# Optimization experiments

Hardware: AMD Instinct MI355X
Metric: run time of the kernel (lower is better)

## Reference

```python
import jax, jax.numpy as jnp
import numpy as np

S = 128            # image_size
NF = 64            # nf (channels)
B, N = 16, 1
DIM = S * S // 16  # 1024
HEADS = max(1, S // 16)  # 8
DH = DIM // HEADS  # 128


def setup_inputs() -> dict:
    key = jax.random.key(0)
    ks = jax.random.split(key, 10)
    sc = lambda fan_in: 1.0 / np.sqrt(fan_in)
    return {
        "x": jax.random.normal(ks[0], (B, N, NF, S, S), dtype=jnp.float32),
        "We": jax.random.uniform(ks[1], (DIM, S * S), jnp.float32, -sc(S * S), sc(S * S)),
        "be": jax.random.uniform(ks[2], (DIM,), jnp.float32, -sc(S * S), sc(S * S)),
        "pos": jax.random.normal(ks[3], (1, NF, DIM), dtype=jnp.float32),
        "Wq": jax.random.uniform(ks[4], (DIM, DIM), jnp.float32, -sc(DIM), sc(DIM)),
        "Wk": jax.random.uniform(ks[5], (NF, NF), jnp.float32, -sc(NF), sc(NF)),
        "Wv": jax.random.uniform(ks[6], (DIM, DIM), jnp.float32, -sc(DIM), sc(DIM)),
        "Wo": jax.random.uniform(ks[7], (S * S, DIM), jnp.float32, -sc(DIM), sc(DIM)),
        "bo": jax.random.uniform(ks[8], (S * S,), jnp.float32, -sc(DIM), sc(DIM)),
    }


def reference(x, We, be, pos, Wq, Wk, Wv, Wo, bo):
    b, n, C, H, W = x.shape
    bn = b * n
    xf = x.reshape(bn, C, H * W)                       # [BN, C, S^2]
    xe = jnp.einsum('bcp,dp->bcd', xf, We) + be + pos  # [BN, C, DIM]
    # q projection -> heads -> avgpool over head dim (AvgPool1d(dh) == mean)
    q = jnp.einsum('bcd,ed->bce', xe, Wq).reshape(bn, C, HEADS, DH)
    q = q.transpose(0, 2, 1, 3)                        # [BN, H, C, dh]
    q = q.mean(axis=-1)                                # [BN, H, C]
    k = jax.nn.sigmoid(jnp.einsum('bhc,fc->bhf', q, Wk))  # [BN, H, C]
    v = jnp.einsum('bcd,ed->bce', xe, Wv).reshape(bn, C, HEADS, DH)
    v = v.transpose(0, 2, 1, 3)                        # [BN, H, C, dh]
    # diag_embed(k) @ v == per-channel elementwise scale
    out = k[..., None] * v                             # [BN, H, C, dh]
    out = out.transpose(0, 2, 1, 3).reshape(bn, C, DIM)
    out = jnp.einsum('bcd,pd->bcp', out, Wo) + bo      # [BN, C, S^2]
    return out.reshape(b, n, C, H, W)
```

## Files before the change

### kernel.cpp

```cpp
#include <hip/hip_runtime.h>
#include <cstdint>
#include <cmath>


typedef __attribute__((ext_vector_type(8))) short short8;
typedef __attribute__((ext_vector_type(4))) float f32x4;

#define DIMD 1024
#define NCH  64
#define NHEAD 8
#define DHEAD 128

typedef __attribute__((address_space(1))) unsigned int gu32;
typedef __attribute__((address_space(3))) unsigned int lu32;

__device__ __forceinline__ void gload_lds16(const void* g, void* l) {
  __builtin_amdgcn_global_load_lds((gu32*)g, (lu32*)l, 16, 0, 0);
}

__device__ __forceinline__ unsigned short f2bf(float f) {
  union { float f; unsigned u; } a; a.f = f;
  unsigned u = a.u;
  unsigned r = (u + 0x7fffu + ((u >> 16) & 1u)) >> 16;
  return (unsigned short)r;
}
__device__ __forceinline__ float bf2f(unsigned short h) {
  union { unsigned u; float f; } a; a.u = ((unsigned)h) << 16; return a.f;
}

__device__ __forceinline__ void cvt8_body(const float* __restrict__ in,
                                          unsigned short* __restrict__ out, int i) {
  const float4* p = (const float4*)in + (size_t)i * 2;
  float4 f0 = p[0], f1 = p[1];
  uint4 u;
  u.x = (unsigned)f2bf(f0.x) | ((unsigned)f2bf(f0.y) << 16);
  u.y = (unsigned)f2bf(f0.z) | ((unsigned)f2bf(f0.w) << 16);
  u.z = (unsigned)f2bf(f1.x) | ((unsigned)f2bf(f1.y) << 16);
  u.w = (unsigned)f2bf(f1.z) | ((unsigned)f2bf(f1.w) << 16);
  ((uint4*)out)[i] = u;
}

__global__ __launch_bounds__(256) void cvt_bf16_kernel(
    const float* __restrict__ in, unsigned short* __restrict__ out, int n8) {
  int i = blockIdx.x * 256 + threadIdx.x;
  if (i >= n8) return;
  cvt8_body(in, out, i);
}

__global__ __launch_bounds__(256) void prep_fused(
    const float* __restrict__ x,  unsigned short* __restrict__ x_bf,
    const float* __restrict__ We, unsigned short* __restrict__ We_bf,
    const float* __restrict__ Wo, unsigned short* __restrict__ Wo_bf,
    const float* __restrict__ Wv, unsigned short* __restrict__ Wv_bf,
    const float* __restrict__ Wq, float* __restrict__ wqm) {
  int b = blockIdx.x;
  if (b < 8192) {
    cvt8_body(x, x_bf, b * 256 + threadIdx.x);
  } else if (b < 16384) {
    cvt8_body(We, We_bf, (b - 8192) * 256 + threadIdx.x);
  } else if (b < 24576) {
    cvt8_body(Wo, Wo_bf, (b - 16384) * 256 + threadIdx.x);
  } else if (b < 25088) {
    cvt8_body(Wv, Wv_bf, (b - 24576) * 256 + threadIdx.x);
  } else {
    int bb = b - 25088;
    int h = bb >> 3, dbase = (bb & 7) * 128;
    int d = threadIdx.x & 127, eh = threadIdx.x >> 7;
    const float* p = Wq + ((size_t)(h * DHEAD + eh * 64)) * DIMD + dbase + d;
    float s = 0.f;
    #pragma unroll 8
    for (int e = 0; e < 64; ++e) s += p[(size_t)e * DIMD];
    __shared__ float red[2][128];
    red[eh][d] = s;
    __syncthreads();
    if (eh == 0)
      wqm[h * DIMD + dbase + d] = (red[0][d] + red[1][d]) * (1.0f / DHEAD);
  }
}

__global__ __launch_bounds__(256) void wqm2_kernel(
    const float* __restrict__ Wq, float* __restrict__ wqm) {
  int h = blockIdx.x >> 3, dbase = (blockIdx.x & 7) * 128;
  int d = threadIdx.x & 127, eh = threadIdx.x >> 7;
  const float* p = Wq + ((size_t)(h * DHEAD + eh * 64)) * DIMD + dbase + d;
  float s = 0.f;
  #pragma unroll 8
  for (int e = 0; e < 64; ++e) s += p[(size_t)e * DIMD];
  __shared__ float red[2][128];
  red[eh][d] = s;
  __syncthreads();
  if (eh == 0)
    wqm[h * DIMD + dbase + d] = (red[0][d] + red[1][d]) * (1.0f / DHEAD);
}

__global__ __launch_bounds__(256) void qk2_kernel(
    const unsigned short* __restrict__ xe, const float* __restrict__ wqm,
    const float* __restrict__ Wk, float* __restrict__ kout) {
  int b = blockIdx.x, h = blockIdx.y;
  int c = threadIdx.x & 63, dq = threadIdx.x >> 6;
  __shared__ float red[64][4];
  __shared__ float qs[64];
  const uint4* xr = (const uint4*)(xe + ((size_t)(b * NCH + c)) * DIMD + dq * 256);
  const float* wr = wqm + h * DIMD + dq * 256;
  float s = 0.f;
  #pragma unroll 4
  for (int i = 0; i < 32; ++i) {
    uint4 v = xr[i];
    s += bf2f((unsigned short)(v.x & 0xffff)) * wr[i * 8 + 0];
    s += bf2f((unsigned short)(v.x >> 16))    * wr[i * 8 + 1];
    s += bf2f((unsigned short)(v.y & 0xffff)) * wr[i * 8 + 2];
    s += bf2f((unsigned short)(v.y >> 16))    * wr[i * 8 + 3];
    s += bf2f((unsigned short)(v.z & 0xffff)) * wr[i * 8 + 4];
    s += bf2f((unsigned short)(v.z >> 16))    * wr[i * 8 + 5];
    s += bf2f((unsigned short)(v.w & 0xffff)) * wr[i * 8 + 6];
    s += bf2f((unsigned short)(v.w >> 16))    * wr[i * 8 + 7];
  }
  red[c][dq] = s;
  __syncthreads();
  if (dq == 0) qs[c] = red[c][0] + red[c][1] + red[c][2] + red[c][3];
  __syncthreads();
  int f = c;
  float s2 = 0.f;
  #pragma unroll
  for (int i = 0; i < 16; ++i) {
    int cc = dq * 16 + i;
    s2 += qs[cc] * Wk[f * NCH + cc];
  }
  red[f][dq] = s2;
  __syncthreads();
  if (dq == 0) {
    float q = red[f][0] + red[f][1] + red[f][2] + red[f][3];
    kout[(b * NHEAD + h) * NCH + f] = 1.f / (1.f + expf(-q));
  }
}


#define BARR asm volatile("s_barrier" ::: "memory")
#define VMW(n) asm volatile("s_waitcnt vmcnt(" #n ")" ::: "memory")
#define ENDPH do { \
  asm volatile("s_waitcnt lgkmcnt(0)" ::: "memory"); \
  __builtin_amdgcn_sched_barrier(0); \
  BARR; } while (0)

#define SA(bb, kk, u) gload_lds16(gA + (size_t)(u) * 64 * K + (kk), \
                                  lA0 + (bb) * 16384 + (u) * 4096)
#define SB(bb, kk, u) gload_lds16(gB + (size_t)(u) * 64 * K + (kk), \
                                  lB0 + (bb) * 16384 + (u) * 4096)

#define PH(QM, QN, LOADA, STG) do { \
  if (LOADA) { \
    const unsigned short* ap = &As[buf][wm * 128 + (QM) * 64 + rl][0]; \
    _Pragma("unroll") \
    for (int i = 0; i < 4; ++i) { \
      af0[i] = *(const short8*)(ap + i * 1024 + ((q ^ swz) << 3)); \
      af1[i] = *(const short8*)(ap + i * 1024 + (((4 | q) ^ swz) << 3)); \
    } \
  } \
  const unsigned short* bp = &Bs[buf][wn * 64 + (QN) * 32 + rl][0]; \
  short8 b00 = *(const short8*)(bp + ((q ^ swz) << 3)); \
  short8 b01 = *(const short8*)(bp + 1024 + ((q ^ swz) << 3)); \
  short8 b10 = *(const short8*)(bp + (((4 | q) ^ swz) << 3)); \
  short8 b11 = *(const short8*)(bp + 1024 + (((4 | q) ^ swz) << 3)); \
  STG; \
  BARR; \
  __builtin_amdgcn_s_setprio(1); \
  _Pragma("unroll") \
  for (int i = 0; i < 4; ++i) { \
    acc[(QM)*4+i][(QN)*2+0] = __builtin_amdgcn_mfma_f32_16x16x32_bf16(af0[i], b00, acc[(QM)*4+i][(QN)*2+0], 0, 0, 0); \
    acc[(QM)*4+i][(QN)*2+0] = __builtin_amdgcn_mfma_f32_16x16x32_bf16(af1[i], b10, acc[(QM)*4+i][(QN)*2+0], 0, 0, 0); \
    acc[(QM)*4+i][(QN)*2+1] = __builtin_amdgcn_mfma_f32_16x16x32_bf16(af0[i], b01, acc[(QM)*4+i][(QN)*2+1], 0, 0, 0); \
    acc[(QM)*4+i][(QN)*2+1] = __builtin_amdgcn_mfma_f32_16x16x32_bf16(af1[i], b11, acc[(QM)*4+i][(QN)*2+1], 0, 0, 0); \
  } \
  __builtin_amdgcn_s_setprio(0); \
  ENDPH; \
} while (0)

template<int MODE, int LAYOUT>
__global__ __launch_bounds__(512, 2) void gemm8(
    const unsigned short* __restrict__ A, const unsigned short* __restrict__ Bg,
    float* __restrict__ C, const float* __restrict__ bias,
    int M, int N, int K, int Ksub)
{
  __shared__ __align__(16) unsigned short As[2][256][64];
  __shared__ __align__(16) unsigned short Bs[2][256][64];

  const int bid = blockIdx.x;
  int m0, n0, kz;
  if (LAYOUT == 1) {
    kz = (bid & 7) | (((bid >> 3) & 1) << 3);
    int r = bid >> 4; n0 = (r & 3) * 256; m0 = (r >> 2) * 256;
  } else {
    int nlo = bid & 7; int r = bid >> 3;
    m0 = (r & 3) * 256; n0 = (nlo + 8 * (r >> 2)) * 256; kz = 0;
  }
  const int kbeg = kz * Ksub;
  const int NT = Ksub >> 6;

  const int tid  = threadIdx.x;
  const int lane = tid & 63, wave = tid >> 6;
  const int wm = wave >> 2, wn = wave & 3;
  const int q = lane >> 4, rl = lane & 15;
  const int swz = rl & 7;

  const int srow = wave * 8 + (lane >> 3);
  const int kswz = ((lane & 7) ^ (lane >> 3)) << 3;
  const unsigned short* gA = A  + (size_t)(m0 + srow) * K + kbeg + kswz;
  const unsigned short* gB = Bg + (size_t)(n0 + srow) * K + kbeg + kswz;
  unsigned short* lA0 = &As[0][0][0] + wave * 512;
  unsigned short* lB0 = &Bs[0][0][0] + wave * 512;

  f32x4 acc[8][4] = {};
  short8 af0[4], af1[4];

  SA(0, 0, 0); SA(0, 0, 2);
  SB(0, 0, 0); SB(0, 0, 1); SB(0, 0, 2); SB(0, 0, 3);
  SA(0, 0, 1); SA(0, 0, 3);
  VMW(2);
  BARR;

  for (int t = 0; t < NT; ++t) {
    const int buf = t & 1;
    const int nb = buf ^ 1;
    const bool s = (t + 1) < NT;
    const size_t kn = (size_t)(t + 1) * 64;

    PH(0, 0, true,  if (s) { SB(nb, kn, 0); SB(nb, kn, 1); });
    PH(0, 1, false, if (s) { SB(nb, kn, 2); SB(nb, kn, 3); VMW(4); } else VMW(0));
    PH(1, 0, true,  if (s) { SA(nb, kn, 0); SA(nb, kn, 2); });
    PH(1, 1, false, if (s) { SA(nb, kn, 1); SA(nb, kn, 3); VMW(2); });
  }

  const size_t zoff = (MODE == 3) ? (size_t)kz * (size_t)M * (size_t)N : 0;
  #pragma unroll
  for (int mi = 0; mi < 8; ++mi) {
    #pragma unroll
    for (int nj = 0; nj < 4; ++nj) {
      #pragma unroll
      for (int r = 0; r < 4; ++r) {
        int row = m0 + wm * 128 + mi * 16 + q * 4 + r;
        int col = n0 + wn * 64 + nj * 16 + rl;
        if (MODE == 3) {
          C[zoff + (size_t)row * N + col] = acc[mi][nj][r];
        } else {
          C[(size_t)row * N + col] = acc[mi][nj][r] + bias[col];
        }
      }
    }
  }
}

template<int MODE, int LAYOUT>
__global__ __launch_bounds__(256) void gemm_db(
    const unsigned short* __restrict__ A, const unsigned short* __restrict__ B,
    float* __restrict__ C, const float* __restrict__ bias,
    int M, int N, int K, int Ksub)
{
  __shared__ __align__(16) unsigned short As[2][128][32];
  __shared__ __align__(16) unsigned short Bs[2][128][32];

  const int bid = blockIdx.x;
  int m0, n0, kz;
  if (LAYOUT == 0) {
    kz = bid & 7; int r = bid >> 3; n0 = (r & 7) * 128; m0 = (r >> 3) * 128;
  } else if (LAYOUT == 1) {
    kz = (bid & 7) | (((bid >> 3) & 1) << 3);
    int r = bid >> 4; n0 = (r & 7) * 128; m0 = (r >> 3) * 128;
  } else {
    int nlo = bid & 7, nhi = bid >> 6;
    m0 = ((bid >> 3) & 7) * 128; n0 = (nlo + 8 * nhi) * 128; kz = 0;
  }

  const int tid  = threadIdx.x;
  const int lane = tid & 63, wave = tid >> 6;
  const int kbeg = kz * Ksub;
  const int lrow = lane >> 2;
  const int lcol = (lane & 3) * 8;
  const int q = lane >> 4, rl = lane & 15;
  const int wr = (wave >> 1) * 64, wc = (wave & 1) * 64;

  const unsigned short* ga = A + (size_t)(m0 + wave * 32 + lrow) * K + kbeg + lcol;
  const unsigned short* gb = B + (size_t)(n0 + wave * 32 + lrow) * K + kbeg + lcol;

  f32x4 acc[4][4] = {};

  gload_lds16(ga,                  &As[0][wave * 32][0]);
  gload_lds16(ga + (size_t)16 * K, &As[0][wave * 32 + 16][0]);
  gload_lds16(gb,                  &Bs[0][wave * 32][0]);
  gload_lds16(gb + (size_t)16 * K, &Bs[0][wave * 32 + 16][0]);
  ga += 32; gb += 32;

  int p = 0;
  for (int k0 = 0; k0 < Ksub; k0 += 32) {
    __syncthreads();
    if (k0 + 32 < Ksub) {
      gload_lds16(ga,                  &As[p ^ 1][wave * 32][0]);
      gload_lds16(ga + (size_t)16 * K, &As[p ^ 1][wave * 32 + 16][0]);
      gload_lds16(gb,                  &Bs[p ^ 1][wave * 32][0]);
      gload_lds16(gb + (size_t)16 * K, &Bs[p ^ 1][wave * 32 + 16][0]);
      ga += 32; gb += 32;
    }

    short8 af[4], bf[4];
    #pragma unroll
    for (int i = 0; i < 4; ++i)
      af[i] = *(const short8*)&As[p][wr + i * 16 + rl][q * 8];
    #pragma unroll
    for (int j = 0; j < 4; ++j)
      bf[j] = *(const short8*)&Bs[p][wc + j * 16 + rl][q * 8];
    #pragma unroll
    for (int i = 0; i < 4; ++i)
      #pragma unroll
      for (int j = 0; j < 4; ++j)
        acc[i][j] = __builtin_amdgcn_mfma_f32_16x16x32_bf16(af[i], bf[j], acc[i][j], 0, 0, 0);

    p ^= 1;
  }

  const size_t zoff = (MODE == 3) ? (size_t)kz * (size_t)M * (size_t)N : 0;
  #pragma unroll
  for (int i = 0; i < 4; ++i) {
    #pragma unroll
    for (int j = 0; j < 4; ++j) {
      #pragma unroll
      for (int r = 0; r < 4; ++r) {
        int row = m0 + wr + i * 16 + q * 4 + r;
        int col = n0 + wc + j * 16 + rl;
        if (MODE == 3) {
          C[zoff + (size_t)row * N + col] = acc[i][j][r];
        } else {
          C[(size_t)row * N + col] = acc[i][j][r] + bias[col];
        }
      }
    }
  }
}

template<int NS>
__global__ __launch_bounds__(256) void reduce1_kernel(
    const float* __restrict__ part, const float* __restrict__ be,
    const float* __restrict__ pos, unsigned short* __restrict__ xe) {
  int i = blockIdx.x * 256 + threadIdx.x;
  size_t base = (size_t)i * 4;
  int row = i >> 8, col = (i & 255) * 4;
  float4 s = {0.f, 0.f, 0.f, 0.f};
  #pragma unroll
  for (int sk = 0; sk < NS; ++sk) {
    float4 p = *(const float4*)(part + (size_t)sk * (DIMD * DIMD) + base);
    s.x += p.x; s.y += p.y; s.z += p.z; s.w += p.w;
  }
  float4 bv = *(const float4*)(be + col);
  float4 pv = *(const float4*)(pos + (size_t)(row & 63) * DIMD + col);
  uint2 u;
  u.x = (unsigned)f2bf(s.x + bv.x + pv.x) | ((unsigned)f2bf(s.y + bv.y + pv.y) << 16);
  u.y = (unsigned)f2bf(s.z + bv.z + pv.z) | ((unsigned)f2bf(s.w + bv.w + pv.w) << 16);
  *(uint2*)(xe + base) = u;
}

template<int NS>
__global__ __launch_bounds__(256) void reduce2_kernel(
    const float* __restrict__ part, const float* __restrict__ kv,
    unsigned short* __restrict__ t) {
  int i = blockIdx.x * 256 + threadIdx.x;
  size_t base = (size_t)i * 4;
  int row = i >> 8, col = (i & 255) * 4;
  float4 s = {0.f, 0.f, 0.f, 0.f};
  #pragma unroll
  for (int sk = 0; sk < NS; ++sk) {
    float4 p = *(const float4*)(part + (size_t)sk * (DIMD * DIMD) + base);
    s.x += p.x; s.y += p.y; s.z += p.z; s.w += p.w;
  }
  float sc = kv[((row >> 6) * NHEAD + (col >> 7)) * NCH + (row & 63)];
  uint2 u;
  u.x = (unsigned)f2bf(s.x * sc) | ((unsigned)f2bf(s.y * sc) << 16);
  u.y = (unsigned)f2bf(s.z * sc) | ((unsigned)f2bf(s.w * sc) << 16);
  *(uint2*)(t + base) = u;
}

template<int MODE, bool ABF16, int BM, int BN>
__global__ __launch_bounds__(256) void gemm_bt(
    const void* __restrict__ Ap, const float* __restrict__ B,
    void* __restrict__ C, const float* __restrict__ bias,
    const float* __restrict__ posp, const float* __restrict__ ksc,
    int M, int N, int K)
{
  constexpr int BK = 32;
  constexpr int LDR = BK + 8;
  __shared__ __align__(16) unsigned short As[BM][LDR];
  __shared__ __align__(16) unsigned short Bs[BN][LDR];

  const int tid = threadIdx.x;
  const int m0 = blockIdx.y * BM;
  const int n0 = blockIdx.x * BN;
  constexpr int EA = BM * BK / 256;
  constexpr int EB = BN * BK / 256;
  constexpr int MI = BM / 32;
  constexpr int NI = BN / 32;
  const int lane = tid & 63, wave = tid >> 6;
  const int wr = (wave >> 1) * (BM / 2);
  const int wc = (wave & 1) * (BN / 2);
  const int q = lane >> 4, rl = lane & 15;

  f32x4 acc[MI][NI] = {};

  for (int k0 = 0; k0 < K; k0 += BK) {
    {
      constexpr int CPR = BK / EA;
      int row = tid / CPR;
      int cs  = (tid % CPR) * EA;
      if (ABF16) {
        const unsigned short* a = (const unsigned short*)Ap + (size_t)(m0 + row) * K + k0 + cs;
        #pragma unroll
        for (int v = 0; v < EA / 8; ++v)
          *(uint4*)&As[row][cs + v * 8] = *(const uint4*)(a + v * 8);
      } else {
        const float* a = (const float*)Ap + (size_t)(m0 + row) * K + k0 + cs;
        #pragma unroll
        for (int v = 0; v < EA / 8; ++v) {
          float4 f0 = *(const float4*)(a + v * 8);
          float4 f1 = *(const float4*)(a + v * 8 + 4);
          uint4 u;
          u.x = (unsigned)f2bf(f0.x) | ((unsigned)f2bf(f0.y) << 16);
          u.y = (unsigned)f2bf(f0.z) | ((unsigned)f2bf(f0.w) << 16);
          u.z = (unsigned)f2bf(f1.x) | ((unsigned)f2bf(f1.y) << 16);
          u.w = (unsigned)f2bf(f1.z) | ((unsigned)f2bf(f1.w) << 16);
          *(uint4*)&As[row][cs + v * 8] = u;
        }
      }
    }
    {
      constexpr int CPR = BK / EB;
      int row = tid / CPR;
      int cs  = (tid % CPR) * EB;
      const float* b = B + (size_t)(n0 + row) * K + k0 + cs;
      #pragma unroll
      for (int v = 0; v < EB / 8; ++v) {
        float4 f0 = *(const float4*)(b + v * 8);
        float4 f1 = *(const float4*)(b + v * 8 + 4);
        uint4 u;
        u.x = (unsigned)f2bf(f0.x) | ((unsigned)f2bf(f0.y) << 16);
        u.y = (unsigned)f2bf(f0.z) | ((unsigned)f2bf(f0.w) << 16);
        u.z = (unsigned)f2bf(f1.x) | ((unsigned)f2bf(f1.y) << 16);
        u.w = (unsigned)f2bf(f1.z) | ((unsigned)f2bf(f1.w) << 16);
        *(uint4*)&Bs[row][cs + v * 8] = u;
      }
    }
    __syncthreads();

    short8 af[MI], bf[NI];
    #pragma unroll
    for (int i = 0; i < MI; ++i)
      af[i] = *(const short8*)&As[wr + i * 16 + rl][q * 8];
    #pragma unroll
    for (int j = 0; j < NI; ++j)
      bf[j] = *(const short8*)&Bs[wc + j * 16 + rl][q * 8];
    #pragma unroll
    for (int i = 0; i < MI; ++i)
      #pragma unroll
      for (int j = 0; j < NI; ++j)
        acc[i][j] = __builtin_amdgcn_mfma_f32_16x16x32_bf16(af[i], bf[j], acc[i][j], 0, 0, 0);

    __syncthreads();
  }

  #pragma unroll
  for (int i = 0; i < MI; ++i) {
    #pragma unroll
    for (int j = 0; j < NI; ++j) {
      #pragma unroll
      for (int r = 0; r < 4; ++r) {
        int row = m0 + wr + i * 16 + q * 4 + r;
        int col = n0 + wc + j * 16 + rl;
        float v = acc[i][j][r];
        if (MODE == 0) {
          v += bias[col] + posp[(size_t)(row & 63) * DIMD + col];
          ((unsigned short*)C)[(size_t)row * N + col] = f2bf(v);
        } else if (MODE == 1) {
          v *= ksc[((row >> 6) * NHEAD + (col >> 7)) * NCH + (row & 63)];
          ((unsigned short*)C)[(size_t)row * N + col] = f2bf(v);
        } else {
          ((float*)C)[(size_t)row * N + col] = v + bias[col];
        }
      }
    }
  }
}

__global__ void wqm_kernel(const float* __restrict__ Wq, float* __restrict__ wqm) {
  int h = blockIdx.x;
  for (int d = threadIdx.x; d < DIMD; d += 256) {
    float s = 0.f;
    const float* p = Wq + (size_t)h * DHEAD * DIMD + d;
    #pragma unroll 4
    for (int e = 0; e < DHEAD; ++e) s += p[(size_t)e * DIMD];
    wqm[h * DIMD + d] = s * (1.0f / DHEAD);
  }
}
__global__ void qk_kernel(const unsigned short* __restrict__ xe,
                          const float* __restrict__ wqm,
                          const float* __restrict__ Wk,
                          float* __restrict__ kout) {
  int b = blockIdx.x;
  __shared__ float qs[NHEAD][NCH];
  for (int t = threadIdx.x; t < NHEAD * NCH; t += 256) {
    int h = t >> 6, c = t & 63;
    const unsigned short* xr = xe + (size_t)(b * NCH + c) * DIMD;
    const float* wr = wqm + h * DIMD;
    float s = 0.f;
    #pragma unroll 8
    for (int d = 0; d < DIMD; ++d) s += bf2f(xr[d]) * wr[d];
    qs[h][c] = s;
  }
  __syncthreads();
  for (int t = threadIdx.x; t < NHEAD * NCH; t += 256) {
    int h = t >> 6, f = t & 63;
    float s = 0.f;
    #pragma unroll
    for (int c = 0; c < NCH; ++c) s += qs[h][c] * Wk[f * NCH + c];
    kout[b * (NHEAD * NCH) + h * NCH + f] = 1.f / (1.f + expf(-s));
  }
}

extern "C" void kernel_launch(void* const* d_in, const int* in_sizes, int n_in,
                              void* d_out, int out_size, void* d_ws, size_t ws_size,
                              hipStream_t stream) {
  const float* x   = (const float*)d_in[0];
  const float* We  = (const float*)d_in[1];
  const float* be  = (const float*)d_in[2];
  const float* pos = (const float*)d_in[3];
  const float* Wq  = (const float*)d_in[4];
  const float* Wk  = (const float*)d_in[5];
  const float* Wv  = (const float*)d_in[6];
  const float* Wo  = (const float*)d_in[7];
  const float* bo  = (const float*)d_in[8];
  float* out = (float*)d_out;

  const size_t MB = 1u << 20;
  const size_t WS16 = 102 * MB + 64 * 1024;
  const size_t WS8  = 70 * MB + 64 * 1024;

  if (ws_size >= WS16) {
    char* ws = (char*)d_ws;
    unsigned short* We_bf = (unsigned short*)(ws + 0);
    unsigned short* Wo_bf = (unsigned short*)(ws + 32 * MB);
    unsigned short* x_bf  = (unsigned short*)(ws + 64 * MB);
    unsigned short* Wv_bf = (unsigned short*)(ws + 96 * MB);
    unsigned short* xe    = (unsigned short*)(ws + 98 * MB);
    unsigned short* t     = (unsigned short*)(ws + 100 * MB);
    float* wqm = (float*)(ws + 102 * MB);
    float* kv  = (float*)(ws + 102 * MB + 32 * 1024);

    float* part1 = (float*)d_out;
    float* part2 = (float*)d_out;

    prep_fused<<<dim3(25152), 256, 0, stream>>>(
        x, x_bf, We, We_bf, Wo, Wo_bf, Wv, Wv_bf, Wq, wqm);

    gemm8<3, 1><<<dim3(256), 512, 0, stream>>>(
        x_bf, We_bf, part1, nullptr, 1024, 1024, 16384, 1024);
    reduce1_kernel<16><<<dim3(1024), 256, 0, stream>>>(part1, be, pos, xe);

    qk2_kernel<<<dim3(16, 8), 256, 0, stream>>>(xe, wqm, Wk, kv);

    gemm_db<3, 0><<<dim3(512), 256, 0, stream>>>(
        xe, Wv_bf, part2, nullptr, 1024, 1024, 1024, 128);
    reduce2_kernel<8><<<dim3(1024), 256, 0, stream>>>(part2, kv, t);

    gemm8<2, 2><<<dim3(256), 512, 0, stream>>>(
        t, Wo_bf, out, bo, 1024, 16384, 1024, 1024);
  } else if (ws_size >= WS8) {
    char* ws = (char*)d_ws;
    unsigned short* We_bf = (unsigned short*)(ws + 0);
    unsigned short* Wo_bf = (unsigned short*)(ws + 32 * MB);
    unsigned short* Wv_bf = (unsigned short*)(ws + 64 * MB);
    unsigned short* xe    = (unsigned short*)(ws + 66 * MB);
    unsigned short* t     = (unsigned short*)(ws + 68 * MB);
    float* wqm = (float*)(ws + 70 * MB);
    float* kv  = (float*)(ws + 70 * MB + 32 * 1024);

    char* ob = (char*)d_out;
    unsigned short* x_bf  = (unsigned short*)(ob + 0);
    float* part1 = (float*)(ob + 32 * MB);
    float* part2 = (float*)(ob + 0);

    cvt_bf16_kernel<<<dim3(8192), 256, 0, stream>>>(x,  x_bf,  16777216 / 8);
    cvt_bf16_kernel<<<dim3(8192), 256, 0, stream>>>(We, We_bf, 16777216 / 8);
    cvt_bf16_kernel<<<dim3(512),  256, 0, stream>>>(Wv, Wv_bf, 1048576 / 8);
    cvt_bf16_kernel<<<dim3(8192), 256, 0, stream>>>(Wo, Wo_bf, 16777216 / 8);
    wqm2_kernel<<<dim3(64), 256, 0, stream>>>(Wq, wqm);

    gemm_db<3, 0><<<dim3(512), 256, 0, stream>>>(
        x_bf, We_bf, part1, nullptr, 1024, 1024, 16384, 2048);
    reduce1_kernel<8><<<dim3(1024), 256, 0, stream>>>(part1, be, pos, xe);

    qk2_kernel<<<dim3(16, 8), 256, 0, stream>>>(xe, wqm, Wk, kv);

    gemm_db<3, 0><<<dim3(512), 256, 0, stream>>>(
        xe, Wv_bf, part2, nullptr, 1024, 1024, 1024, 128);
    reduce2_kernel<8><<<dim3(1024), 256, 0, stream>>>(part2, kv, t);

    gemm_db<2, 2><<<dim3(1024), 256, 0, stream>>>(
        t, Wo_bf, out, bo, 1024, 16384, 1024, 1024);
  } else {
    char* ws = (char*)d_ws;
    unsigned short* xe = (unsigned short*)ws;
    unsigned short* t  = (unsigned short*)(ws + (2u << 20));
    float* wqm = (float*)(ws + (4u << 20));
    float* kv  = (float*)(ws + (4u << 20) + (32u << 10));

    wqm_kernel<<<dim3(NHEAD), 256, 0, stream>>>(Wq, wqm);
    gemm_bt<0, false, 64, 64><<<dim3(16, 16), 256, 0, stream>>>(
        x, We, xe, be, pos, nullptr, 1024, 1024, 16384);
    qk_kernel<<<dim3(16), 256, 0, stream>>>(xe, wqm, Wk, kv);
    gemm_bt<1, true, 64, 64><<<dim3(16, 16), 256, 0, stream>>>(
        xe, Wv, t, nullptr, nullptr, kv, 1024, 1024, 1024);
    gemm_bt<2, true, 128, 128><<<dim3(128, 8), 256, 0, stream>>>(
        t, Wo, out, bo, nullptr, nullptr, 1024, 16384, 1024);
  }
}
```

Before: 350.2 us.

## Restructure gemm8 main loop to single barrier per K-tile with bulk prefetch

Replaces the four-phase ping-pong schedule in gemm8 with a simpler loop. At the start of each K-tile it issues all next-tile global-to-LDS loads, then runs two half-K MFMA sweeps over the full 8x4 accumulator tile, and ends with one vmcnt wait and one barrier. This removes three barriers per iteration and the fine-grained interleaving of loads and compute. It also holds more fragment registers at once and gives up the staggered overlap between waves that the phased schedule provided. The bf16 packing code is moved into a pack8 helper, which is a pure cleanup.

```diff
diff --git a/kernel.cpp b/kernel.cpp
--- a/kernel.cpp
+++ b/kernel.cpp
@@ -28,16 +28,19 @@
   union { unsigned u; float f; } a; a.u = ((unsigned)h) << 16; return a.f;
 }
 
-__device__ __forceinline__ void cvt8_body(const float* __restrict__ in,
-                                          unsigned short* __restrict__ out, int i) {
-  const float4* p = (const float4*)in + (size_t)i * 2;
-  float4 f0 = p[0], f1 = p[1];
+__device__ __forceinline__ uint4 pack8(float4 f0, float4 f1) {
   uint4 u;
   u.x = (unsigned)f2bf(f0.x) | ((unsigned)f2bf(f0.y) << 16);
   u.y = (unsigned)f2bf(f0.z) | ((unsigned)f2bf(f0.w) << 16);
   u.z = (unsigned)f2bf(f1.x) | ((unsigned)f2bf(f1.y) << 16);
   u.w = (unsigned)f2bf(f1.z) | ((unsigned)f2bf(f1.w) << 16);
-  ((uint4*)out)[i] = u;
+  return u;
+}
+
+__device__ __forceinline__ void cvt8_body(const float* __restrict__ in,
+                                          unsigned short* __restrict__ out, int i) {
+  const float4* p = (const float4*)in + (size_t)i * 2;
+  ((uint4*)out)[i] = pack8(p[0], p[1]);
 }
 
 __global__ __launch_bounds__(256) void cvt_bf16_kernel(
@@ -137,43 +140,12 @@
 
 #define BARR asm volatile("s_barrier" ::: "memory")
 #define VMW(n) asm volatile("s_waitcnt vmcnt(" #n ")" ::: "memory")
-#define ENDPH do { \
-  asm volatile("s_waitcnt lgkmcnt(0)" ::: "memory"); \
-  __builtin_amdgcn_sched_barrier(0); \
-  BARR; } while (0)
+#define LGKM0 asm volatile("s_waitcnt lgkmcnt(0)" ::: "memory")
 
 #define SA(bb, kk, u) gload_lds16(gA + (size_t)(u) * 64 * K + (kk), \
                                   lA0 + (bb) * 16384 + (u) * 4096)
 #define SB(bb, kk, u) gload_lds16(gB + (size_t)(u) * 64 * K + (kk), \
                                   lB0 + (bb) * 16384 + (u) * 4096)
-
-#define PH(QM, QN, LOADA, STG) do { \
-  if (LOADA) { \
-    const unsigned short* ap = &As[buf][wm * 128 + (QM) * 64 + rl][0]; \
-    _Pragma("unroll") \
-    for (int i = 0; i < 4; ++i) { \
-      af0[i] = *(const short8*)(ap + i * 1024 + ((q ^ swz) << 3)); \
-      af1[i] = *(const short8*)(ap + i * 1024 + (((4 | q) ^ swz) << 3)); \
-    } \
-  } \
-  const unsigned short* bp = &Bs[buf][wn * 64 + (QN) * 32 + rl][0]; \
-  short8 b00 = *(const short8*)(bp + ((q ^ swz) << 3)); \
-  short8 b01 = *(const short8*)(bp + 1024 + ((q ^ swz) << 3)); \
-  short8 b10 = *(const short8*)(bp + (((4 | q) ^ swz) << 3)); \
-  short8 b11 = *(const short8*)(bp + 1024 + (((4 | q) ^ swz) << 3)); \
-  STG; \
-  BARR; \
-  __builtin_amdgcn_s_setprio(1); \
-  _Pragma("unroll") \
-  for (int i = 0; i < 4; ++i) { \
-    acc[(QM)*4+i][(QN)*2+0] = __builtin_amdgcn_mfma_f32_16x16x32_bf16(af0[i], b00, acc[(QM)*4+i][(QN)*2+0], 0, 0, 0); \
-    acc[(QM)*4+i][(QN)*2+0] = __builtin_amdgcn_mfma_f32_16x16x32_bf16(af1[i], b10, acc[(QM)*4+i][(QN)*2+0], 0, 0, 0); \
-    acc[(QM)*4+i][(QN)*2+1] = __builtin_amdgcn_mfma_f32_16x16x32_bf16(af0[i], b01, acc[(QM)*4+i][(QN)*2+1], 0, 0, 0); \
-    acc[(QM)*4+i][(QN)*2+1] = __builtin_amdgcn_mfma_f32_16x16x32_bf16(af1[i], b11, acc[(QM)*4+i][(QN)*2+1], 0, 0, 0); \
-  } \
-  __builtin_amdgcn_s_setprio(0); \
-  ENDPH; \
-} while (0)
 
 template<int MODE, int LAYOUT>
 __global__ __launch_bounds__(512, 2) void gemm8(
@@ -210,24 +182,62 @@
   unsigned short* lB0 = &Bs[0][0][0] + wave * 512;
 
   f32x4 acc[8][4] = {};
-  short8 af0[4], af1[4];
-
-  SA(0, 0, 0); SA(0, 0, 2);
+
+  SA(0, 0, 0); SA(0, 0, 1); SA(0, 0, 2); SA(0, 0, 3);
   SB(0, 0, 0); SB(0, 0, 1); SB(0, 0, 2); SB(0, 0, 3);
-  SA(0, 0, 1); SA(0, 0, 3);
-  VMW(2);
+  VMW(0);
   BARR;
 
+  const int g0 = (q ^ swz) << 3;
+  const int g1 = ((4 | q) ^ swz) << 3;
+
   for (int t = 0; t < NT; ++t) {
-    const int buf = t & 1;
-    const int nb = buf ^ 1;
-    const bool s = (t + 1) < NT;
-    const size_t kn = (size_t)(t + 1) * 64;
-
-    PH(0, 0, true,  if (s) { SB(nb, kn, 0); SB(nb, kn, 1); });
-    PH(0, 1, false, if (s) { SB(nb, kn, 2); SB(nb, kn, 3); VMW(4); } else VMW(0));
-    PH(1, 0, true,  if (s) { SA(nb, kn, 0); SA(nb, kn, 2); });
-    PH(1, 1, false, if (s) { SA(nb, kn, 1); SA(nb, kn, 3); VMW(2); });
+    const int buf = t & 1, nb = buf ^ 1;
+    if (t + 1 < NT) {
+      const size_t kn = (size_t)(t + 1) * 64;
+      SA(nb, kn, 0); SA(nb, kn, 1); SA(nb, kn, 2); SA(nb, kn, 3);
+      SB(nb, kn, 0); SB(nb, kn, 1); SB(nb, kn, 2); SB(nb, kn, 3);
+    }
+    const unsigned short* ap = &As[buf][wm * 128 + rl][0];
+    const unsigned short* bp = &Bs[buf][wn * 64 + rl][0];
+
+    short8 a0[8], b0[4];
+    #pragma unroll
+    for (int mi = 0; mi < 8; ++mi)
+      a0[mi] = *(const short8*)(ap + mi * 1024 + g0);
+    #pragma unroll
+    for (int nj = 0; nj < 4; ++nj)
+      b0[nj] = *(const short8*)(bp + nj * 1024 + g0);
+    LGKM0;
+    __builtin_amdgcn_sched_barrier(0);
+    __builtin_amdgcn_s_setprio(1);
+    #pragma unroll
+    for (int mi = 0; mi < 8; ++mi)
+      #pragma unroll
+      for (int nj = 0; nj < 4; ++nj)
+        acc[mi][nj] = __builtin_amdgcn_mfma_f32_16x16x32_bf16(a0[mi], b0[nj], acc[mi][nj], 0, 0, 0);
+    __builtin_amdgcn_s_setprio(0);
+
+    short8 a1[8], b1[4];
+    #pragma unroll
+    for (int mi = 0; mi < 8; ++mi)
+      a1[mi] = *(const short8*)(ap + mi * 1024 + g1);
+    #pragma unroll
+    for (int nj = 0; nj < 4; ++nj)
+      b1[nj] = *(const short8*)(bp + nj * 1024 + g1);
+    LGKM0;
+    __builtin_amdgcn_sched_barrier(0);
+    __builtin_amdgcn_s_setprio(1);
+    #pragma unroll
+    for (int mi = 0; mi < 8; ++mi)
+      #pragma unroll
+      for (int nj = 0; nj < 4; ++nj)
+        acc[mi][nj] = __builtin_amdgcn_mfma_f32_16x16x32_bf16(a1[mi], b1[nj], acc[mi][nj], 0, 0, 0);
+    __builtin_amdgcn_s_setprio(0);
+
+    VMW(0);
+    __builtin_amdgcn_sched_barrier(0);
+    BARR;
   }
 
   const size_t zoff = (MODE == 3) ? (size_t)kz * (size_t)M * (size_t)N : 0;
@@ -418,12 +428,7 @@
         for (int v = 0; v < EA / 8; ++v) {
           float4 f0 = *(const float4*)(a + v * 8);
           float4 f1 = *(const float4*)(a + v * 8 + 4);
-          uint4 u;
-          u.x = (unsigned)f2bf(f0.x) | ((unsigned)f2bf(f0.y) << 16);
-          u.y = (unsigned)f2bf(f0.z) | ((unsigned)f2bf(f0.w) << 16);
-          u.z = (unsigned)f2bf(f1.x) | ((unsigned)f2bf(f1.y) << 16);
-          u.w = (unsigned)f2bf(f1.z) | ((unsigned)f2bf(f1.w) << 16);
-          *(uint4*)&As[row][cs + v * 8] = u;
+          *(uint4*)&As[row][cs + v * 8] = pack8(f0, f1);
         }
       }
     }
@@ -436,12 +441,7 @@
       for (int v = 0; v < EB / 8; ++v) {
         float4 f0 = *(const float4*)(b + v * 8);
         float4 f1 = *(const float4*)(b + v * 8 + 4);
-        uint4 u;
-        u.x = (unsigned)f2bf(f0.x) | ((unsigned)f2bf(f0.y) << 16);
-        u.y = (unsigned)f2bf(f0.z) | ((unsigned)f2bf(f0.w) << 16);
-        u.z = (unsigned)f2bf(f1.x) | ((unsigned)f2bf(f1.y) << 16);
-        u.w = (unsigned)f2bf(f1.z) | ((unsigned)f2bf(f1.w) << 16);
-        *(uint4*)&Bs[row][cs + v * 8] = u;
+        *(uint4*)&Bs[row][cs + v * 8] = pack8(f0, f1);
       }
     }
     __syncthreads();
```

New measurement: 354.8 us. No clear change (+1.3%).
